# Optimization experiments

Measured on AMD Instinct MI355X. Metric: run time of the kernel, lower is better.

Reference implementation:

```python
import jax, jax.numpy as jnp
import numpy as np


def setup_inputs() -> dict:
    key = jax.random.key(0)
    k1, k2 = jax.random.split(key)
    x = jax.random.normal(k1, (8, 128, 128, 128), dtype=jnp.float32)        # [N, C, H, W]
    codebook = jax.random.normal(k2, (256, 128), dtype=jnp.float32)         # [K, C] class_emb_vecs
    return {"x": x, "codebook": codebook}


def reference(x, codebook):
    # Brute-force 1-NN with p=2 (Euclidean), matching sklearn NearestNeighbors(brute, p=2).
    # argmin ||q - c||_2 == argmin (||q||^2 - 2 q.c + ||c||^2), so use the GEMM form.
    N, C, H, W = x.shape
    q = jnp.transpose(x, (0, 2, 3, 1)).reshape(-1, C)       # [N*H*W, C], matches x.reshape(-1, C) channel-last? 
    # NOTE: torch x.reshape(-1, C) on [N,C,H,W] flattens with C as the fastest-varying of the
    # leading dims only when memory layout is NCHW -> rows are (n, c_blocks)... Torch's
    # reshape(-1, C) actually slices contiguous groups of C elements along W. To be faithful
    # to x.reshape(-1, C) on a contiguous NCHW tensor:
    q = x.reshape(-1, C)                                     # [N*C*H*W/C, C] — same elements, same order as torch
    q_sq = jnp.sum(q * q, axis=1, keepdims=True)             # [M, 1]
    c_sq = jnp.sum(codebook * codebook, axis=1)              # [K]
    # squared distances: [M, K]
    d2 = q_sq - 2.0 * (q @ codebook.T) + c_sq[None, :]
    idx = jnp.argmin(d2, axis=1).astype(jnp.int32)           # [M]
    return idx.reshape(N, H, W)
```

## Files before the change

kernel.cpp:

```cpp
#include <hip/hip_runtime.h>
#include <hip/hip_bf16.h>


typedef __bf16 bf16x8 __attribute__((ext_vector_type(8)));
typedef float  floatx4 __attribute__((ext_vector_type(4)));

#define MFMA16 __builtin_amdgcn_mfma_f32_16x16x32_bf16

#define CNT_OFF 0
#define CSQ_OFF 1024
#define CBB_OFF 4096
#define WL_OFF  (4096 + 131072)
#define WL_CAP  32768
#define T_FLAG  0.004f

typedef __attribute__((address_space(1))) const unsigned int gu32;
typedef __attribute__((address_space(3))) unsigned int lu32;

__device__ __forceinline__ unsigned fmap(float f) {
    unsigned u = __float_as_uint(f);
    return (u & 0x80000000u) ? ~u : (u | 0x80000000u);
}

__global__ void knn_prep(const float* __restrict__ cb, __bf16* __restrict__ cbB,
                         float* __restrict__ csq, int* __restrict__ cnt) {
    const int tid = threadIdx.x;
    const int id = blockIdx.x * 256 + tid;
    if (id == 0) *cnt = 0;
    const int ln = id & 63;
    const int part = (id >> 6) & 1;
    const int step = id >> 7;
    const int t4 = step & 15;
    const int kb = step >> 4;
    const int n = t4 * 16 + (ln & 15);
    const int k0 = kb * 32 + (ln >> 4) * 8;
    const float* src = cb + (size_t)n * 128 + k0;
    union { __bf16 h[8]; uint4 u; } p;
#pragma unroll
    for (int j = 0; j < 8; ++j) {
        float f = src[j];
        __bf16 hh = (__bf16)f;
        p.h[j] = (part == 0) ? hh : (__bf16)(f - (float)hh);
    }
    *(uint4*)(cbB + (size_t)id * 8) = p.u;

    if (blockIdx.x == 0) {
        const float4* row = (const float4*)(cb + (size_t)tid * 128);
        float a0 = 0.f, a1 = 0.f, a2 = 0.f, a3 = 0.f;
#pragma unroll 8
        for (int j = 0; j < 32; ++j) {
            float4 v = row[j];
            a0 = fmaf(v.x, v.x, a0);
            a1 = fmaf(v.y, v.y, a1);
            a2 = fmaf(v.z, v.z, a2);
            a3 = fmaf(v.w, v.w, a3);
        }
        csq[tid] = (a0 + a1) + (a2 + a3);
    }
}

__global__ __launch_bounds__(512, 2) void knn_mfma(const float* __restrict__ x,
                                                   const __bf16* __restrict__ cbB,
                                                   const float* __restrict__ csq_g,
                                                   int* __restrict__ out,
                                                   int* __restrict__ cnt,
                                                   int* __restrict__ wl) {
    __shared__ __bf16 sB[65536];

    const int tid = threadIdx.x;
    const int wave = tid >> 6;
    const int lane = tid & 63;
    const int rl = lane & 15;
    const int kg = lane >> 4;

    {
        const char* gsrc = (const char*)cbB + wave * 16384 + lane * 16;
        char* ldst = (char*)sB + wave * 16384;
#pragma unroll
        for (int i = 0; i < 16; ++i)
            __builtin_amdgcn_global_load_lds((gu32*)(gsrc + i * 1024),
                                             (lu32*)(ldst + i * 1024), 16, 0, 0);
    }

    float cs[16];
#pragma unroll
    for (int t = 0; t < 16; ++t) cs[t] = csq_g[t * 16 + rl];

#pragma unroll 1
    for (int bt = 0; bt < 2; ++bt) {
        const int be = bt ^ ((wave >> 2) & 1);
        const size_t q0 = ((size_t)blockIdx.x * 2 + be) * 256 + wave * 32;

        const float* xq = x + q0 * 128;
        bf16x8 ah[2][4], al[2][4];
#pragma unroll
        for (int m = 0; m < 2; ++m) {
#pragma unroll
            for (int kb = 0; kb < 4; ++kb) {
                const float* s = xq + (size_t)(m * 16 + rl) * 128 + kb * 32 + kg * 8;
                float4 f0 = *(const float4*)(s);
                float4 f1 = *(const float4*)(s + 4);
                float f[8] = {f0.x, f0.y, f0.z, f0.w, f1.x, f1.y, f1.z, f1.w};
                union { __bf16 h[8]; bf16x8 v; } ph, pl;
#pragma unroll
                for (int j = 0; j < 8; ++j) {
                    __bf16 hh = (__bf16)f[j];
                    ph.h[j] = hh;
                    pl.h[j] = (__bf16)(f[j] - (float)hh);
                }
                ah[m][kb] = ph.v;
                al[m][kb] = pl.v;
            }
        }

        floatx4 acc[2][16];
#pragma unroll
        for (int m = 0; m < 2; ++m)
#pragma unroll
            for (int t = 0; t < 16; ++t) acc[m][t] = (floatx4){0.f, 0.f, 0.f, 0.f};

        if (bt == 0) __syncthreads();

#pragma unroll
        for (int kb = 0; kb < 4; ++kb) {
            const __bf16* sbase = sB + kb * 16384 + lane * 8;
#pragma unroll
            for (int t = 0; t < 16; ++t) {
                bf16x8 bh = *(const bf16x8*)(sbase + t * 1024);
                bf16x8 bl = *(const bf16x8*)(sbase + t * 1024 + 512);
                acc[0][t] = MFMA16(ah[0][kb], bh, acc[0][t], 0, 0, 0);
                acc[1][t] = MFMA16(ah[1][kb], bh, acc[1][t], 0, 0, 0);
                acc[0][t] = MFMA16(al[0][kb], bh, acc[0][t], 0, 0, 0);
                acc[1][t] = MFMA16(al[1][kb], bh, acc[1][t], 0, 0, 0);
                acc[0][t] = MFMA16(ah[0][kb], bl, acc[0][t], 0, 0, 0);
                acc[1][t] = MFMA16(ah[1][kb], bl, acc[1][t], 0, 0, 0);
            }
        }

#pragma unroll
        for (int m = 0; m < 2; ++m) {
#pragma unroll
            for (int r = 0; r < 4; ++r) {
                float bf = __builtin_inff(), sf = __builtin_inff();
                int bi = 0;
#pragma unroll
                for (int t = 0; t < 16; ++t) {
                    const float sc = fmaf(-2.0f, acc[m][t][r], cs[t]);
                    const bool lt = sc < bf;
                    sf = lt ? bf : fminf(sf, sc);
                    bf = lt ? sc : bf;
                    bi = lt ? (t * 16 + rl) : bi;
                }
#pragma unroll
                for (int d = 1; d < 16; d <<= 1) {
                    const float obf = __shfl_xor(bf, d);
                    const int   obi = __shfl_xor(bi, d);
                    const float osf = __shfl_xor(sf, d);
                    const bool lt = obf < bf;
                    const float loser = lt ? bf : obf;
                    sf = fminf(fminf(sf, osf), loser);
                    bf = lt ? obf : bf;
                    bi = lt ? obi : bi;
                }
                if (rl == 0) {
                    const size_t qg = q0 + m * 16 + kg * 4 + r;
                    out[qg] = bi;
                    if (sf - bf < T_FLAG) {
                        int idx = atomicAdd(cnt, 1);
                        if (idx < WL_CAP) wl[idx] = (int)qg;
                    }
                }
            }
        }
    }
}

__global__ __launch_bounds__(256) void knn_refine(const float* __restrict__ x,
                                                  const float* __restrict__ cb,
                                                  const float* __restrict__ csq_g,
                                                  const int* __restrict__ wl,
                                                  const int* __restrict__ cnt,
                                                  int* __restrict__ out) {
    __shared__ unsigned long long sP[4];
    const int tid = threadIdx.x;
    const int lane = tid & 63;
    const int wave = tid >> 6;

    int n = *cnt;
    if (n > WL_CAP) n = WL_CAP;
    const float mycsq = csq_g[tid];
    const float4* cr = (const float4*)(cb + (size_t)tid * 128);

    for (int i = blockIdx.x; i < n; i += gridDim.x) {
        const int q = wl[i];
        const float4* qr = (const float4*)(x + (size_t)q * 128);
        float a0 = 0.f, a1 = 0.f, a2 = 0.f, a3 = 0.f;
#pragma unroll 8
        for (int c4 = 0; c4 < 32; ++c4) {
            float4 qv = qr[c4];
            float4 cv = cr[c4];
            a0 = fmaf(qv.x, cv.x, a0);
            a1 = fmaf(qv.y, cv.y, a1);
            a2 = fmaf(qv.z, cv.z, a2);
            a3 = fmaf(qv.w, cv.w, a3);
        }
        float dot = (a0 + a1) + (a2 + a3);
        float score = fmaf(-2.0f, dot, mycsq);
        unsigned long long key =
            ((unsigned long long)fmap(score) << 32) | (unsigned)tid;
#pragma unroll
        for (int d = 1; d < 64; d <<= 1) {
            unsigned long long o = __shfl_xor(key, d);
            key = o < key ? o : key;
        }
        if (lane == 0) sP[wave] = key;
        __syncthreads();
        if (tid == 0) {
            unsigned long long b = sP[0];
            unsigned long long o;
            o = sP[1]; b = o < b ? o : b;
            o = sP[2]; b = o < b ? o : b;
            o = sP[3]; b = o < b ? o : b;
            out[q] = (int)(unsigned)(b & 0xFFFFFFFFull);
        }
        __syncthreads();
    }
}

extern "C" void kernel_launch(void* const* d_in, const int* in_sizes, int n_in,
                              void* d_out, int out_size, void* d_ws, size_t ws_size,
                              hipStream_t stream) {
    const float* x = (const float*)d_in[0];
    const float* cb = (const float*)d_in[1];
    int* out = (int*)d_out;

    char* ws = (char*)d_ws;
    int* cnt = (int*)(ws + CNT_OFF);
    float* csq = (float*)(ws + CSQ_OFF);
    __bf16* cbB = (__bf16*)(ws + CBB_OFF);
    int* wl = (int*)(ws + WL_OFF);

    const int M = in_sizes[0] / 128;

    knn_prep<<<32, 256, 0, stream>>>(cb, cbB, csq, cnt);
    knn_mfma<<<M / 512, 512, 0, stream>>>(x, cbB, csq, out, cnt, wl);
    knn_refine<<<240, 256, 0, stream>>>(x, cb, csq, wl, cnt, out);
}
```

Baseline: 148.4 us.

## Shrink per-wave query tile to 16 rows and loop four batches per block

Each wave now handles one 16-row query tile per iteration instead of two, and the block runs four iterations over 128 queries each rather than two over 256. The interleaved batch ordering between wave halves is dropped. Halving the accumulator and A-fragment arrays lowers register pressure, which may raise occupancy. The cost is that each B fragment read from LDS now feeds half as many MFMAs, so LDS traffic per FLOP doubles and the loop overhead is higher.

```diff
diff --git a/kernel.cpp b/kernel.cpp
--- a/kernel.cpp
+++ b/kernel.cpp
@@ -87,37 +87,31 @@
     for (int t = 0; t < 16; ++t) cs[t] = csq_g[t * 16 + rl];
 
 #pragma unroll 1
-    for (int bt = 0; bt < 2; ++bt) {
-        const int be = bt ^ ((wave >> 2) & 1);
-        const size_t q0 = ((size_t)blockIdx.x * 2 + be) * 256 + wave * 32;
+    for (int bt = 0; bt < 4; ++bt) {
+        const size_t q0 = (size_t)blockIdx.x * 512 + bt * 128 + wave * 16;
 
         const float* xq = x + q0 * 128;
-        bf16x8 ah[2][4], al[2][4];
-#pragma unroll
-        for (int m = 0; m < 2; ++m) {
-#pragma unroll
-            for (int kb = 0; kb < 4; ++kb) {
-                const float* s = xq + (size_t)(m * 16 + rl) * 128 + kb * 32 + kg * 8;
-                float4 f0 = *(const float4*)(s);
-                float4 f1 = *(const float4*)(s + 4);
-                float f[8] = {f0.x, f0.y, f0.z, f0.w, f1.x, f1.y, f1.z, f1.w};
-                union { __bf16 h[8]; bf16x8 v; } ph, pl;
-#pragma unroll
-                for (int j = 0; j < 8; ++j) {
-                    __bf16 hh = (__bf16)f[j];
-                    ph.h[j] = hh;
-                    pl.h[j] = (__bf16)(f[j] - (float)hh);
-                }
-                ah[m][kb] = ph.v;
-                al[m][kb] = pl.v;
-            }
-        }
-
-        floatx4 acc[2][16];
-#pragma unroll
-        for (int m = 0; m < 2; ++m)
-#pragma unroll
-            for (int t = 0; t < 16; ++t) acc[m][t] = (floatx4){0.f, 0.f, 0.f, 0.f};
+        bf16x8 ah[4], al[4];
+#pragma unroll
+        for (int kb = 0; kb < 4; ++kb) {
+            const float* s = xq + (size_t)rl * 128 + kb * 32 + kg * 8;
+            float4 f0 = *(const float4*)(s);
+            float4 f1 = *(const float4*)(s + 4);
+            float f[8] = {f0.x, f0.y, f0.z, f0.w, f1.x, f1.y, f1.z, f1.w};
+            union { __bf16 h[8]; bf16x8 v; } ph, pl;
+#pragma unroll
+            for (int j = 0; j < 8; ++j) {
+                __bf16 hh = (__bf16)f[j];
+                ph.h[j] = hh;
+                pl.h[j] = (__bf16)(f[j] - (float)hh);
+            }
+            ah[kb] = ph.v;
+            al[kb] = pl.v;
+        }
+
+        floatx4 acc[16];
+#pragma unroll
+        for (int t = 0; t < 16; ++t) acc[t] = (floatx4){0.f, 0.f, 0.f, 0.f};
 
         if (bt == 0) __syncthreads();
 
@@ -128,47 +122,41 @@
             for (int t = 0; t < 16; ++t) {
                 bf16x8 bh = *(const bf16x8*)(sbase + t * 1024);
                 bf16x8 bl = *(const bf16x8*)(sbase + t * 1024 + 512);
-                acc[0][t] = MFMA16(ah[0][kb], bh, acc[0][t], 0, 0, 0);
-                acc[1][t] = MFMA16(ah[1][kb], bh, acc[1][t], 0, 0, 0);
-                acc[0][t] = MFMA16(al[0][kb], bh, acc[0][t], 0, 0, 0);
-                acc[1][t] = MFMA16(al[1][kb], bh, acc[1][t], 0, 0, 0);
-                acc[0][t] = MFMA16(ah[0][kb], bl, acc[0][t], 0, 0, 0);
-                acc[1][t] = MFMA16(ah[1][kb], bl, acc[1][t], 0, 0, 0);
-            }
-        }
-
-#pragma unroll
-        for (int m = 0; m < 2; ++m) {
-#pragma unroll
-            for (int r = 0; r < 4; ++r) {
-                float bf = __builtin_inff(), sf = __builtin_inff();
-                int bi = 0;
-#pragma unroll
-                for (int t = 0; t < 16; ++t) {
-                    const float sc = fmaf(-2.0f, acc[m][t][r], cs[t]);
-                    const bool lt = sc < bf;
-                    sf = lt ? bf : fminf(sf, sc);
-                    bf = lt ? sc : bf;
-                    bi = lt ? (t * 16 + rl) : bi;
-                }
-#pragma unroll
-                for (int d = 1; d < 16; d <<= 1) {
-                    const float obf = __shfl_xor(bf, d);
-                    const int   obi = __shfl_xor(bi, d);
-                    const float osf = __shfl_xor(sf, d);
-                    const bool lt = obf < bf;
-                    const float loser = lt ? bf : obf;
-                    sf = fminf(fminf(sf, osf), loser);
-                    bf = lt ? obf : bf;
-                    bi = lt ? obi : bi;
-                }
-                if (rl == 0) {
-                    const size_t qg = q0 + m * 16 + kg * 4 + r;
-                    out[qg] = bi;
-                    if (sf - bf < T_FLAG) {
-                        int idx = atomicAdd(cnt, 1);
-                        if (idx < WL_CAP) wl[idx] = (int)qg;
-                    }
+                acc[t] = MFMA16(ah[kb], bh, acc[t], 0, 0, 0);
+                acc[t] = MFMA16(al[kb], bh, acc[t], 0, 0, 0);
+                acc[t] = MFMA16(ah[kb], bl, acc[t], 0, 0, 0);
+            }
+        }
+
+#pragma unroll
+        for (int r = 0; r < 4; ++r) {
+            float bf = __builtin_inff(), sf = __builtin_inff();
+            int bi = 0;
+#pragma unroll
+            for (int t = 0; t < 16; ++t) {
+                const float sc = fmaf(-2.0f, acc[t][r], cs[t]);
+                const bool lt = sc < bf;
+                sf = lt ? bf : fminf(sf, sc);
+                bf = lt ? sc : bf;
+                bi = lt ? (t * 16 + rl) : bi;
+            }
+#pragma unroll
+            for (int d = 1; d < 16; d <<= 1) {
+                const float obf = __shfl_xor(bf, d);
+                const int   obi = __shfl_xor(bi, d);
+                const float osf = __shfl_xor(sf, d);
+                const bool lt = obf < bf;
+                const float loser = lt ? bf : obf;
+                sf = fminf(fminf(sf, osf), loser);
+                bf = lt ? obf : bf;
+                bi = lt ? obi : bi;
+            }
+            if (rl == 0) {
+                const size_t qg = q0 + kg * 4 + r;
+                out[qg] = bi;
+                if (sf - bf < T_FLAG) {
+                    int idx = atomicAdd(cnt, 1);
+                    if (idx < WL_CAP) wl[idx] = (int)qg;
                 }
             }
         }
```

Measured after the change: 121.9 us. -17.8%, faster.

## Split codebook columns across wave pairs and merge argmin through LDS

Applied to the files above, without the earlier changes.

Each pair of waves now shares one 32-query tile, and each wave covers half of the 256 codebook entries. This halves the accumulator and csq registers per wave and doubles the number of tile iterations. Per-wave best, second-best and index are written to shared memory, and after a block barrier one wave per pair merges the two halves and emits the output and flag. The aim is lower register pressure, possibly higher occupancy, at the cost of an extra __syncthreads per iteration, loading A-fragments twice, and a serialized merge step.

```diff
diff --git a/kernel.cpp b/kernel.cpp
--- a/kernel.cpp
+++ b/kernel.cpp
@@ -66,12 +66,17 @@
                                                    int* __restrict__ cnt,
                                                    int* __restrict__ wl) {
     __shared__ __bf16 sB[65536];
+    __shared__ float sBF[2][4][2][32];
+    __shared__ float sSF[2][4][2][32];
+    __shared__ int   sBI[2][4][2][32];
 
     const int tid = threadIdx.x;
     const int wave = tid >> 6;
     const int lane = tid & 63;
     const int rl = lane & 15;
     const int kg = lane >> 4;
+    const int pair = wave >> 1;
+    const int half = wave & 1;
 
     {
         const char* gsrc = (const char*)cbB + wave * 16384 + lane * 16;
@@ -82,14 +87,14 @@
                                              (lu32*)(ldst + i * 1024), 16, 0, 0);
     }
 
-    float cs[16];
-#pragma unroll
-    for (int t = 0; t < 16; ++t) cs[t] = csq_g[t * 16 + rl];
+    float cs[8];
+#pragma unroll
+    for (int t = 0; t < 8; ++t) cs[t] = csq_g[(half * 8 + t) * 16 + rl];
 
 #pragma unroll 1
-    for (int bt = 0; bt < 2; ++bt) {
-        const int be = bt ^ ((wave >> 2) & 1);
-        const size_t q0 = ((size_t)blockIdx.x * 2 + be) * 256 + wave * 32;
+    for (int bt = 0; bt < 4; ++bt) {
+        const int bb = bt & 1;
+        const size_t q0 = (size_t)blockIdx.x * 512 + bt * 128 + pair * 32;
 
         const float* xq = x + q0 * 128;
         bf16x8 ah[2][4], al[2][4];
@@ -113,19 +118,19 @@
             }
         }
 
-        floatx4 acc[2][16];
+        floatx4 acc[2][8];
 #pragma unroll
         for (int m = 0; m < 2; ++m)
 #pragma unroll
-            for (int t = 0; t < 16; ++t) acc[m][t] = (floatx4){0.f, 0.f, 0.f, 0.f};
+            for (int t = 0; t < 8; ++t) acc[m][t] = (floatx4){0.f, 0.f, 0.f, 0.f};
 
         if (bt == 0) __syncthreads();
 
 #pragma unroll
         for (int kb = 0; kb < 4; ++kb) {
-            const __bf16* sbase = sB + kb * 16384 + lane * 8;
-#pragma unroll
-            for (int t = 0; t < 16; ++t) {
+            const __bf16* sbase = sB + kb * 16384 + half * 8192 + lane * 8;
+#pragma unroll
+            for (int t = 0; t < 8; ++t) {
                 bf16x8 bh = *(const bf16x8*)(sbase + t * 1024);
                 bf16x8 bl = *(const bf16x8*)(sbase + t * 1024 + 512);
                 acc[0][t] = MFMA16(ah[0][kb], bh, acc[0][t], 0, 0, 0);
@@ -144,12 +149,12 @@
                 float bf = __builtin_inff(), sf = __builtin_inff();
                 int bi = 0;
 #pragma unroll
-                for (int t = 0; t < 16; ++t) {
+                for (int t = 0; t < 8; ++t) {
                     const float sc = fmaf(-2.0f, acc[m][t][r], cs[t]);
                     const bool lt = sc < bf;
                     sf = lt ? bf : fminf(sf, sc);
                     bf = lt ? sc : bf;
-                    bi = lt ? (t * 16 + rl) : bi;
+                    bi = lt ? ((half * 8 + t) * 16 + rl) : bi;
                 }
 #pragma unroll
                 for (int d = 1; d < 16; d <<= 1) {
@@ -163,13 +168,30 @@
                     bi = lt ? obi : bi;
                 }
                 if (rl == 0) {
-                    const size_t qg = q0 + m * 16 + kg * 4 + r;
-                    out[qg] = bi;
-                    if (sf - bf < T_FLAG) {
-                        int idx = atomicAdd(cnt, 1);
-                        if (idx < WL_CAP) wl[idx] = (int)qg;
-                    }
-                }
+                    const int ql = m * 16 + kg * 4 + r;
+                    sBF[bb][pair][half][ql] = bf;
+                    sSF[bb][pair][half][ql] = sf;
+                    sBI[bb][pair][half][ql] = bi;
+                }
+            }
+        }
+
+        __syncthreads();
+
+        if (half == ((pair >> 1) & 1) && lane < 32) {
+            const float b0 = sBF[bb][pair][0][lane];
+            const float b1 = sBF[bb][pair][1][lane];
+            const float s0 = sSF[bb][pair][0][lane];
+            const float s1 = sSF[bb][pair][1][lane];
+            const int   i0 = sBI[bb][pair][0][lane];
+            const int   i1 = sBI[bb][pair][1][lane];
+            const bool w0 = b0 < b1;
+            const float B = w0 ? b0 : b1;
+            const float S = fminf(w0 ? s0 : s1, w0 ? b1 : b0);
+            out[q0 + lane] = w0 ? i0 : i1;
+            if (S - B < T_FLAG) {
+                int idx = atomicAdd(cnt, 1);
+                if (idx < WL_CAP) wl[idx] = (int)(q0 + lane);
             }
         }
     }
```

Measured after the change: 136.3 us. 1.09x faster.
